# Optimization experiments

Measured on AMD Instinct MI355X. Metric: run time of the kernel, lower is better.

Reference implementation:

```python
import jax, jax.numpy as jnp
import numpy as np

CONF_THRES = 0.8
NMS_THRES = 0.4
MAX_DET = 300          # fixed capacity for jit-compatible NMS output
N_BOXES = 262144
N_CLASSES = 80


def xywh2xyxy(x):
    xy, wh = x[..., :2], x[..., 2:4]
    return jnp.concatenate([xy - wh * 0.5, xy + wh * 0.5], axis=-1)


def bbox_iou(box, boxes):
    # one box [4] vs many [N,4]; original uses the +1 pixel-area convention
    x1 = jnp.maximum(box[0], boxes[:, 0])
    y1 = jnp.maximum(box[1], boxes[:, 1])
    x2 = jnp.minimum(box[2], boxes[:, 2])
    y2 = jnp.minimum(box[3], boxes[:, 3])
    inter = jnp.clip(x2 - x1 + 1, 0) * jnp.clip(y2 - y1 + 1, 0)
    a1 = (box[2] - box[0] + 1) * (box[3] - box[1] + 1)
    a2 = (boxes[:, 2] - boxes[:, 0] + 1) * (boxes[:, 3] - boxes[:, 1] + 1)
    return inter / (a1 + a2 - inter + 1e-16)


def nms_single(pred):
    # pred: [N, 85] raw YOLO output for one image
    boxes = xywh2xyxy(pred[:, :4])
    obj = pred[:, 4]
    cls_scores = pred[:, 5:]
    class_conf = cls_scores.max(axis=-1)
    class_pred = jnp.argmax(cls_scores, axis=-1).astype(pred.dtype)
    valid = obj >= CONF_THRES
    score = obj * class_conf
    # sort valid boxes by descending score; invalid pushed to the end
    order = jnp.argsort(jnp.where(valid, -score, jnp.inf))
    det = jnp.concatenate(
        [boxes, obj[:, None], class_conf[:, None], class_pred[:, None]], axis=1
    )[order]  # [N, 7] = x1,y1,x2,y2,obj,class_conf,class_pred
    valid = valid[order]

    def step(valid, _):
        idx = jnp.argmax(valid)            # first still-valid (= highest score)
        any_valid = jnp.any(valid)
        cur = det[idx]
        iou = bbox_iou(cur[:4], det[:, :4])
        invalid = (iou > NMS_THRES) & (det[:, 6] == cur[6]) & valid
        # weighted box merge over the suppressed group (as in original NMS)
        w = jnp.where(invalid, det[:, 4], 0.0)
        merged = (w[:, None] * det[:, :4]).sum(0) / (w.sum() + 1e-16)
        out = jnp.where(any_valid,
                        jnp.concatenate([merged, cur[4:]]),
                        jnp.zeros(7, pred.dtype))
        return valid & ~invalid, (out, any_valid)

    _, (kept, kept_valid) = jax.lax.scan(step, valid, None, length=MAX_DET)
    return kept, kept_valid  # [MAX_DET,7], [MAX_DET]


def setup_inputs() -> dict:
    key = jax.random.key(0)
    detections = jax.random.uniform(key, (1, N_BOXES, 5 + N_CLASSES), dtype=jnp.float32)
    return {"detections": detections}


def reference(detections):
    kept, kv = nms_single(detections[0])
    d = kept[:, 5:]                        # [MAX_DET, 2] = (class_conf, class_pred)
    conf_key = jnp.where(kv, d[:, 0], -jnp.inf)  # padded rows sort to the end
    order = jnp.argsort(conf_key)          # ascending (torch argsort)
    d = d[order][::-1]                     # torch.flip -> descending class_conf
    kv = kv[order][::-1]
    probs = jnp.where(kv, d[:, 0], 0.0)    # self.probs
    ids = d[:, 1][None, :]                 # self.ids, shape [1, MAX_DET]
    return ids, probs
```

## Files before the change

kernel.cpp:

```cpp
#include <hip/hip_runtime.h>

#pragma clang fp contract(off)

#define NBOX 262144
#define NCLS 80
#define ROWS 85
#define CAP 1024
#define NSUB 8
#define SUBCAP 128
#define POOL 8192
#define BPT 2
#define S1BOX 512

typedef unsigned long long ull;

__global__ __launch_bounds__(1024) void k_init(int* __restrict__ cnt_pad,
                                               int* __restrict__ pool_count,
                                               int* __restrict__ done_count) {
    const int t = threadIdx.x;
    for (int i = t; i < NCLS * NSUB * 16; i += 1024) cnt_pad[i] = 0;
    if (t == 0) { *pool_count = 0; *done_count = 0; }
}

__global__ __launch_bounds__(256) void k_stage1(const float* __restrict__ det,
                                                int* __restrict__ cnt_pad,
                                                ull* __restrict__ key2,
                                                float* __restrict__ conf2,
                                                float4* __restrict__ box2) {
    __shared__ int s_wl[S1BOX];
    __shared__ float s_obj[S1BOX];
    __shared__ int s_nv;
    const int t = threadIdx.x;
    const int b0 = blockIdx.x * S1BOX;
    const int sb = blockIdx.x & (NSUB - 1);

    if (t == 0) s_nv = 0;
    __syncthreads();

    float obj[BPT];
    #pragma unroll
    for (int i = 0; i < BPT; i++)
        obj[i] = det[(size_t)(b0 + (i << 8) + t) * ROWS + 4];
    #pragma unroll
    for (int i = 0; i < BPT; i++) {
        if (obj[i] >= 0.8f) {
            int r = atomicAdd(&s_nv, 1);
            s_wl[r] = (i << 8) + t;
            s_obj[r] = obj[i];
        }
    }
    __syncthreads();
    const int nv = s_nv;

    const int grp = t >> 4, c = t & 15;
    const int lane = t & 63;
    #pragma unroll 2
    for (int r0 = 0; r0 < nv; r0 += 16) {
        int widx = r0 + grp;
        if (widx < nv) {
            int b = s_wl[widx];
            const float* p = det + (size_t)(b0 + b) * ROWS;
            float aux = (c < 5) ? p[c] : 0.0f;
            float v0 = p[5 + c];
            float v1 = p[21 + c];
            float v2 = p[37 + c];
            float v3 = p[53 + c];
            float v4 = p[69 + c];
            float mv = v0; int mj = c;
            if (v1 > mv) { mv = v1; mj = 16 + c; }
            if (v2 > mv) { mv = v2; mj = 32 + c; }
            if (v3 > mv) { mv = v3; mj = 48 + c; }
            if (v4 > mv) { mv = v4; mj = 64 + c; }
            #pragma unroll
            for (int off = 8; off; off >>= 1) {
                float ov = __shfl_xor(mv, off);
                int oj = __shfl_xor(mj, off);
                if (ov > mv || (ov == mv && oj < mj)) { mv = ov; mj = oj; }
            }
            int gb = lane & 48;
            float x = __shfl(aux, gb + 0);
            float y = __shfl(aux, gb + 1);
            float w = __shfl(aux, gb + 2);
            float h = __shfl(aux, gb + 3);
            if (c == 0) {
                float ob = s_obj[widx];
                float score = ob * mv;
                float hw = w * 0.5f, hh = h * 0.5f;
                int gi = b0 + b;
                int r = atomicAdd(&cnt_pad[((mj * NSUB + sb) << 4)], 1);
                if (r < SUBCAP) {
                    int pos = (mj << 10) + (sb << 7) + r;
                    key2[pos] = ((ull)(~__float_as_uint(score)) << 32) | (unsigned)gi;
                    conf2[pos] = mv;
                    box2[pos] = make_float4(x - hw, y - hh, x + hw, y + hh);
                }
            }
        }
    }
}

__device__ __forceinline__ int exact_alive16(ull (&k)[16]) {
    int a = 0;
    #pragma unroll
    for (int j = 0; j < 16; j++) a += (int)__popcll(__ballot(k[j] != ~0ULL));
    return a;
}

__device__ __forceinline__ void bsort512(ull (&x)[8], int lane) {
    #pragma unroll
    for (int k = 2; k <= 512; k <<= 1) {
        #pragma unroll
        for (int j = k >> 1; j >= 64; j >>= 1) {
            const int jr = j >> 6;
            #pragma unroll
            for (int r2 = 0; r2 < 8; r2++) {
                if ((r2 & jr) == 0) {
                    const bool asc = (((r2 << 6) & k) == 0);
                    ull a = x[r2], b = x[r2 | jr];
                    if ((a > b) == asc) { x[r2] = b; x[r2 | jr] = a; }
                }
            }
        }
        #pragma unroll
        for (int j = ((k >> 1) > 32 ? 32 : (k >> 1)); j >= 1; j >>= 1) {
            #pragma unroll
            for (int r2 = 0; r2 < 8; r2++) {
                int i = (r2 << 6) + lane;
                bool asc = ((i & k) == 0);
                ull o = __shfl_xor(x[r2], j);
                bool lower = ((lane & j) == 0);
                ull mn = x[r2] < o ? x[r2] : o;
                ull mx2 = x[r2] < o ? o : x[r2];
                x[r2] = (asc == lower) ? mn : mx2;
            }
        }
    }
}

__global__ __launch_bounds__(256) void k_nmsfinal(const int* __restrict__ cnt_pad,
                                                  const ull* __restrict__ key2,
                                                  const float* __restrict__ conf2,
                                                  const float4* __restrict__ box2,
                                                  ull* __restrict__ pool_key,
                                                  float* __restrict__ pool_conf,
                                                  int* __restrict__ pool_cls,
                                                  int* __restrict__ pool_count,
                                                  int* __restrict__ done_count,
                                                  float* __restrict__ out) {
    __shared__ float s_x1[CAP], s_y1[CAP], s_x2[CAP], s_y2[CAP];
    __shared__ float s_area[CAP], s_conf[CAP];
    __shared__ ull s_key[CAP];
    __shared__ int s_cnt[NSUB];
    __shared__ ull pkey[304];
    __shared__ float pconf[304];
    __shared__ int s_fin;
    __shared__ int s_hist[256];
    __shared__ int s_wt[4];
    __shared__ int s_stat[4];
    __shared__ ull s_buf[512];
    __shared__ unsigned s_cb[512];
    __shared__ unsigned s_cl[512];

    const int c = blockIdx.x, t = threadIdx.x, lane = t & 63, wave = t >> 6;
    const int s0 = c << 10;

    ull rk[4]; float4 rb[4]; float rc[4];
    #pragma unroll
    for (int i = 0; i < 4; i++) {
        int pos = t + (i << 8);
        rk[i] = key2[s0 + pos];
        rb[i] = box2[s0 + pos];
        rc[i] = conf2[s0 + pos];
    }
    if (t < NSUB) s_cnt[t] = min(cnt_pad[((c * NSUB + t) << 4)], SUBCAP);
    __syncthreads();
    #pragma unroll
    for (int i = 0; i < 4; i++) {
        int pos = t + (i << 8);
        bool ok = (pos & (SUBCAP - 1)) < s_cnt[pos >> 7];
        float4 b = ok ? rb[i] : make_float4(0.f, 0.f, 0.f, 0.f);
        s_key[pos] = ok ? rk[i] : ~0ULL;
        s_x1[pos] = b.x; s_y1[pos] = b.y; s_x2[pos] = b.z; s_y2[pos] = b.w;
        s_area[pos] = (b.z - b.x + 1.0f) * (b.w - b.y + 1.0f);
        s_conf[pos] = ok ? rc[i] : 0.0f;
    }
    __syncthreads();

    if (wave == 0) {
        int cv0 = 0;
        if (lane < NSUB) cv0 = s_cnt[lane];
        int ntot = cv0;
        #pragma unroll
        for (int off = 32; off; off >>= 1) ntot += __shfl_xor(ntot, off);

        ull k16[16];
        #pragma unroll
        for (int j = 0; j < 16; j++) k16[j] = s_key[(j << 6) + lane];

        int alive = ntot, np = 0;
        while (alive > 0 && np < 300) {
            ull v8[8]; int i8[8];
            #pragma unroll
            for (int j = 0; j < 8; j++) {
                bool l = k16[j + 8] < k16[j];
                v8[j] = l ? k16[j + 8] : k16[j];
                i8[j] = l ? j + 8 : j;
            }
            #pragma unroll
            for (int j = 0; j < 4; j++) {
                if (v8[j + 4] < v8[j]) { v8[j] = v8[j + 4]; i8[j] = i8[j + 4]; }
            }
            if (v8[2] < v8[0]) { v8[0] = v8[2]; i8[0] = i8[2]; }
            if (v8[3] < v8[1]) { v8[1] = v8[3]; i8[1] = i8[3]; }
            if (v8[1] < v8[0]) { v8[0] = v8[1]; i8[0] = i8[1]; }
            ull lm = v8[0]; const int lj = i8[0];

            unsigned lo = (unsigned)lm;
            unsigned hi = (unsigned)(lm >> 32);
            unsigned mh = hi;
            #pragma unroll
            for (int off = 32; off; off >>= 1) {
                unsigned o = __shfl_xor(mh, off);
                mh = o < mh ? o : mh;
            }
            ull wb = __ballot(hi == mh);
            ull gm; int wl2;
            if (mh == 0xFFFFFFFFu || __popcll(wb) != 1) {
                ull g = (hi == mh) ? lm : ~0ULL;
                #pragma unroll
                for (int off = 32; off; off >>= 1) {
                    ull o = __shfl_xor(g, off);
                    if (o < g) g = o;
                }
                gm = g;
                if (gm == ~0ULL) { alive = 0; break; }
                wb = __ballot(lm == gm);
                wl2 = (int)__ffsll((long long)wb) - 1;
            } else {
                wl2 = (int)__ffsll((long long)wb) - 1;
                gm = ((ull)mh << 32) | (ull)__shfl(lo, wl2);
            }
            int wpos = __shfl((lj << 6) + lane, wl2);
            float cx1 = s_x1[wpos], cy1 = s_y1[wpos];
            float cx2 = s_x2[wpos], cy2 = s_y2[wpos];
            float a1 = s_area[wpos];
            if (lane == 0) { pkey[np] = gm; pconf[np] = s_conf[wpos]; }
            np++;
            #pragma unroll
            for (int j = 0; j < 16; j++) {
                if (k16[j] != ~0ULL) {
                    int pos = (j << 6) + lane;
                    float xx1 = fmaxf(cx1, s_x1[pos]), yy1 = fmaxf(cy1, s_y1[pos]);
                    float xx2 = fminf(cx2, s_x2[pos]), yy2 = fminf(cy2, s_y2[pos]);
                    float iw = xx2 - xx1 + 1.0f, ih = yy2 - yy1 + 1.0f;
                    float inter = fmaxf(iw, 0.0f) * fmaxf(ih, 0.0f);
                    float iou = inter / (a1 + s_area[pos] - inter + 1e-16f);
                    if (iou > 0.4f) k16[j] = ~0ULL;
                }
            }
            if ((np & 7) == 0) alive = exact_alive16(k16);
        }

        int npw = min(np, 300);
        int base = 0;
        if (lane == 0 && npw) base = atomicAdd(pool_count, npw);
        base = __shfl(base, 0);
        for (int j = lane; j < npw; j += 64) {
            int pp = base + j;
            if (pp < POOL) {
                ull gm = pkey[j];
                ull pk = ((ull)((unsigned)(gm >> 32) & 0x7FFFFFFFu) << 32)
                       | ((gm & 0xFFFFFFFFull) << 14) | (ull)pp;
                __hip_atomic_store(&pool_key[pp], pk,
                                   __ATOMIC_RELAXED, __HIP_MEMORY_SCOPE_AGENT);
                __hip_atomic_store(&pool_conf[pp], pconf[j],
                                   __ATOMIC_RELAXED, __HIP_MEMORY_SCOPE_AGENT);
                __hip_atomic_store(&pool_cls[pp], c,
                                   __ATOMIC_RELAXED, __HIP_MEMORY_SCOPE_AGENT);
            }
        }
        asm volatile("s_waitcnt vmcnt(0)" ::: "memory");
    }
    __syncthreads();
    if (t == 0) {
        int ticket = atomicAdd(done_count, 1);
        s_fin = (ticket == NCLS - 1) ? 1 : 0;
    }
    __syncthreads();
    if (!s_fin) return;

    const int K = min(__hip_atomic_load(pool_count, __ATOMIC_RELAXED,
                                        __HIP_MEMORY_SCOPE_AGENT), POOL);
    ull key[32];
    #pragma unroll
    for (int j = 0; j < 32; j++) {
        int pos = t + (j << 8);
        key[j] = (pos < K) ? __hip_atomic_load(&pool_key[pos], __ATOMIC_RELAXED,
                                               __HIP_MEMORY_SCOPE_AGENT)
                           : ~0ULL;
    }

    const bool selAll = (K <= 511);
    int sh = 55;
    ull pfin = 0;
    if (!selAll) {
        ull p = 0;
        int gBelow = 0, r = 300;
        while (true) {
            s_hist[t] = 0;
            __syncthreads();
            #pragma unroll
            for (int j = 0; j < 32; j++) {
                ull kk = key[j];
                if ((kk >> (sh + 8)) == p)
                    atomicAdd(&s_hist[(int)((kk >> sh) & 0xFFull)], 1);
            }
            __syncthreads();
            int v = s_hist[t];
            int incv = v;
            for (int off = 1; off < 64; off <<= 1) {
                int o = __shfl_up(incv, off);
                if (lane >= off) incv += o;
            }
            if (lane == 63) s_wt[wave] = incv;
            __syncthreads();
            int wo = 0;
            #pragma unroll
            for (int w2 = 0; w2 < 4; w2++) if (w2 < wave) wo += s_wt[w2];
            int cumIncl = wo + incv;
            int cumExcl = cumIncl - v;
            if (cumExcl < r && r <= cumIncl) {
                s_stat[0] = t; s_stat[1] = cumExcl; s_stat[2] = cumIncl;
            }
            __syncthreads();
            int D = s_stat[0], below = s_stat[1], incl = s_stat[2];
            if (gBelow + incl <= 511 || sh == 7) {
                pfin = (p << 8) | (ull)D;
                break;
            }
            p = (p << 8) | (ull)D;
            gBelow += below;
            r = 300 - gBelow;
            sh -= 8;
            __syncthreads();
        }
    }

    if (t == 0) s_stat[3] = 0;
    __syncthreads();
    int ci = 0;
    #pragma unroll
    for (int j = 0; j < 32; j++) {
        ull kk = key[j];
        bool sel = selAll ? ((kk >> 63) == 0) : ((kk >> sh) <= pfin);
        if (sel) ci++;
    }
    int inc = ci;
    for (int off = 1; off < 64; off <<= 1) {
        int o = __shfl_up(inc, off);
        if (lane >= off) inc += o;
    }
    int wtot = __shfl(inc, 63);
    int wbase2 = 0;
    if (lane == 0 && wtot) wbase2 = atomicAdd(&s_stat[3], wtot);
    wbase2 = __shfl(wbase2, 0);
    int wp = wbase2 + inc - ci;
    #pragma unroll
    for (int j = 0; j < 32; j++) {
        ull kk = key[j];
        bool sel = selAll ? ((kk >> 63) == 0) : ((kk >> sh) <= pfin);
        if (sel) s_buf[wp++] = kk;
    }
    __syncthreads();
    const int S = s_stat[3];
    for (int i = t; i < 512; i += 256) if (i >= S) s_buf[i] = ~0ULL;
    __syncthreads();
    if (wave != 0) return;

    #pragma clang loop unroll(disable)
    for (int pass = 0; pass < 2; pass++) {
        ull x[8];
        #pragma unroll
        for (int r2 = 0; r2 < 8; r2++) x[r2] = s_buf[(r2 << 6) + lane];
        bsort512(x, lane);
        if (pass == 0) {
            #pragma unroll
            for (int r2 = 0; r2 < 8; r2++) {
                int i = (r2 << 6) + lane;
                ull kk = x[r2];
                ull k2 = ~0ULL;
                if (i < 300 && kk != ~0ULL) {
                    int pidx = (int)(kk & 0x3FFFull);
                    unsigned cb = __float_as_uint(
                        __hip_atomic_load(&pool_conf[pidx], __ATOMIC_RELAXED,
                                          __HIP_MEMORY_SCOPE_AGENT));
                    unsigned cl = (unsigned)__hip_atomic_load(&pool_cls[pidx],
                                          __ATOMIC_RELAXED, __HIP_MEMORY_SCOPE_AGENT);
                    s_cb[i] = cb; s_cl[i] = cl;
                    k2 = ((ull)(~cb) << 32) | (unsigned)(~i);
                }
                s_buf[i] = k2;
            }
        } else {
            #pragma unroll
            for (int r2 = 0; r2 < 8; r2++) {
                int i = (r2 << 6) + lane;
                if (i < 300) {
                    ull kk = x[r2];
                    float idv = 0.0f, pv = 0.0f;
                    if (kk != ~0ULL) {
                        int slot = (int)(~(unsigned)(kk & 0xFFFFFFFFull));
                        pv = __uint_as_float(s_cb[slot]);
                        idv = (float)(int)s_cl[slot];
                    }
                    out[i] = idv;
                    out[300 + i] = pv;
                }
            }
        }
    }
}

extern "C" void kernel_launch(void* const* d_in, const int* in_sizes, int n_in,
                              void* d_out, int out_size, void* d_ws, size_t ws_size,
                              hipStream_t stream) {
    const float* det = (const float*)d_in[0];
    float* out = (float*)d_out;
    char* ws = (char*)d_ws;

    int* cnt_pad = (int*)(ws + 0);
    int* pool_count = (int*)(ws + 40960);
    int* done_count = (int*)(ws + 40964);
    ull* key2 = (ull*)(ws + 41024);
    float* conf2 = (float*)(ws + 696384);
    float4* box2 = (float4*)(ws + 1024064);
    ull* pool_key = (ull*)(ws + 2334784);
    float* pool_conf = (float*)(ws + 2400320);
    int* pool_cls = (int*)(ws + 2433088);

    k_init<<<1, 1024, 0, stream>>>(cnt_pad, pool_count, done_count);
    k_stage1<<<NBOX / S1BOX, 256, 0, stream>>>(det, cnt_pad, key2, conf2, box2);
    k_nmsfinal<<<NCLS, 256, 0, stream>>>(cnt_pad, key2, conf2, box2,
                                         pool_key, pool_conf, pool_cls, pool_count,
                                         done_count, out);
}
```

Before: 178.2 us.

## Spread per-class greedy NMS across all four waves with register-resident boxes

The per-class greedy NMS loop, which previously ran on a single wave over 1024 candidates held in shared memory, now runs on all four waves. Each lane keeps four candidates' keys and boxes in registers, and waves exchange their local winners through shared memory every iteration. This cuts per-wave IoU work fourfold and removes the shared-memory box arrays. In exchange, each iteration pays two block-wide barriers. The periodic alive-count check is dropped, so the loop ends when the block minimum becomes the sentinel.

```diff
diff --git a/kernel.cpp b/kernel.cpp
--- a/kernel.cpp
+++ b/kernel.cpp
@@ -99,13 +99,6 @@
     }
 }
 
-__device__ __forceinline__ int exact_alive16(ull (&k)[16]) {
-    int a = 0;
-    #pragma unroll
-    for (int j = 0; j < 16; j++) a += (int)__popcll(__ballot(k[j] != ~0ULL));
-    return a;
-}
-
 __device__ __forceinline__ void bsort512(ull (&x)[8], int lane) {
     #pragma unroll
     for (int k = 2; k <= 512; k <<= 1) {
@@ -147,13 +140,13 @@
                                                   int* __restrict__ pool_count,
                                                   int* __restrict__ done_count,
                                                   float* __restrict__ out) {
-    __shared__ float s_x1[CAP], s_y1[CAP], s_x2[CAP], s_y2[CAP];
-    __shared__ float s_area[CAP], s_conf[CAP];
-    __shared__ ull s_key[CAP];
     __shared__ int s_cnt[NSUB];
+    __shared__ ull s_wkey[4];
+    __shared__ float s_wbox[4][6];
+    __shared__ int s_base;
+    __shared__ int s_fin;
     __shared__ ull pkey[304];
     __shared__ float pconf[304];
-    __shared__ int s_fin;
     __shared__ int s_hist[256];
     __shared__ int s_wt[4];
     __shared__ int s_stat[4];
@@ -164,123 +157,109 @@
     const int c = blockIdx.x, t = threadIdx.x, lane = t & 63, wave = t >> 6;
     const int s0 = c << 10;
 
-    ull rk[4]; float4 rb[4]; float rc[4];
-    #pragma unroll
-    for (int i = 0; i < 4; i++) {
-        int pos = t + (i << 8);
-        rk[i] = key2[s0 + pos];
-        rb[i] = box2[s0 + pos];
-        rc[i] = conf2[s0 + pos];
+    ull k4[4]; float x1[4], y1[4], x2[4], y2[4], ar[4], cf[4];
+    #pragma unroll
+    for (int j = 0; j < 4; j++) {
+        int pos = (wave << 8) + (j << 6) + lane;
+        k4[j] = key2[s0 + pos];
+        float4 b = box2[s0 + pos];
+        x1[j] = b.x; y1[j] = b.y; x2[j] = b.z; y2[j] = b.w;
+        cf[j] = conf2[s0 + pos];
     }
     if (t < NSUB) s_cnt[t] = min(cnt_pad[((c * NSUB + t) << 4)], SUBCAP);
     __syncthreads();
     #pragma unroll
-    for (int i = 0; i < 4; i++) {
-        int pos = t + (i << 8);
+    for (int j = 0; j < 4; j++) {
+        int pos = (wave << 8) + (j << 6) + lane;
         bool ok = (pos & (SUBCAP - 1)) < s_cnt[pos >> 7];
-        float4 b = ok ? rb[i] : make_float4(0.f, 0.f, 0.f, 0.f);
-        s_key[pos] = ok ? rk[i] : ~0ULL;
-        s_x1[pos] = b.x; s_y1[pos] = b.y; s_x2[pos] = b.z; s_y2[pos] = b.w;
-        s_area[pos] = (b.z - b.x + 1.0f) * (b.w - b.y + 1.0f);
-        s_conf[pos] = ok ? rc[i] : 0.0f;
-    }
-    __syncthreads();
-
-    if (wave == 0) {
-        int cv0 = 0;
-        if (lane < NSUB) cv0 = s_cnt[lane];
-        int ntot = cv0;
-        #pragma unroll
-        for (int off = 32; off; off >>= 1) ntot += __shfl_xor(ntot, off);
-
-        ull k16[16];
-        #pragma unroll
-        for (int j = 0; j < 16; j++) k16[j] = s_key[(j << 6) + lane];
-
-        int alive = ntot, np = 0;
-        while (alive > 0 && np < 300) {
-            ull v8[8]; int i8[8];
-            #pragma unroll
-            for (int j = 0; j < 8; j++) {
-                bool l = k16[j + 8] < k16[j];
-                v8[j] = l ? k16[j + 8] : k16[j];
-                i8[j] = l ? j + 8 : j;
-            }
-            #pragma unroll
-            for (int j = 0; j < 4; j++) {
-                if (v8[j + 4] < v8[j]) { v8[j] = v8[j + 4]; i8[j] = i8[j + 4]; }
-            }
-            if (v8[2] < v8[0]) { v8[0] = v8[2]; i8[0] = i8[2]; }
-            if (v8[3] < v8[1]) { v8[1] = v8[3]; i8[1] = i8[3]; }
-            if (v8[1] < v8[0]) { v8[0] = v8[1]; i8[0] = i8[1]; }
-            ull lm = v8[0]; const int lj = i8[0];
-
-            unsigned lo = (unsigned)lm;
-            unsigned hi = (unsigned)(lm >> 32);
-            unsigned mh = hi;
+        if (!ok) {
+            k4[j] = ~0ULL;
+            x1[j] = 0.f; y1[j] = 0.f; x2[j] = 0.f; y2[j] = 0.f; cf[j] = 0.f;
+        }
+        ar[j] = (x2[j] - x1[j] + 1.0f) * (y2[j] - y1[j] + 1.0f);
+    }
+
+    int np = 0;
+    while (np < 300) {
+        ull va = k4[0]; int ia = 0;
+        if (k4[1] < va) { va = k4[1]; ia = 1; }
+        ull vb = k4[2]; int ib = 2;
+        if (k4[3] < vb) { vb = k4[3]; ib = 3; }
+        ull lm = va; int lj = ia;
+        if (vb < va) { lm = vb; lj = ib; }
+        unsigned lo = (unsigned)lm;
+        unsigned hi = (unsigned)(lm >> 32);
+        unsigned mh = hi;
+        #pragma unroll
+        for (int off = 32; off; off >>= 1) {
+            unsigned o = __shfl_xor(mh, off);
+            mh = o < mh ? o : mh;
+        }
+        ull wb = __ballot(hi == mh);
+        ull wm; int wl;
+        if (__popcll(wb) != 1) {
+            ull g = (hi == mh) ? lm : ~0ULL;
             #pragma unroll
             for (int off = 32; off; off >>= 1) {
-                unsigned o = __shfl_xor(mh, off);
-                mh = o < mh ? o : mh;
-            }
-            ull wb = __ballot(hi == mh);
-            ull gm; int wl2;
-            if (mh == 0xFFFFFFFFu || __popcll(wb) != 1) {
-                ull g = (hi == mh) ? lm : ~0ULL;
-                #pragma unroll
-                for (int off = 32; off; off >>= 1) {
-                    ull o = __shfl_xor(g, off);
-                    if (o < g) g = o;
-                }
-                gm = g;
-                if (gm == ~0ULL) { alive = 0; break; }
-                wb = __ballot(lm == gm);
-                wl2 = (int)__ffsll((long long)wb) - 1;
-            } else {
-                wl2 = (int)__ffsll((long long)wb) - 1;
-                gm = ((ull)mh << 32) | (ull)__shfl(lo, wl2);
-            }
-            int wpos = __shfl((lj << 6) + lane, wl2);
-            float cx1 = s_x1[wpos], cy1 = s_y1[wpos];
-            float cx2 = s_x2[wpos], cy2 = s_y2[wpos];
-            float a1 = s_area[wpos];
-            if (lane == 0) { pkey[np] = gm; pconf[np] = s_conf[wpos]; }
-            np++;
-            #pragma unroll
-            for (int j = 0; j < 16; j++) {
-                if (k16[j] != ~0ULL) {
-                    int pos = (j << 6) + lane;
-                    float xx1 = fmaxf(cx1, s_x1[pos]), yy1 = fmaxf(cy1, s_y1[pos]);
-                    float xx2 = fminf(cx2, s_x2[pos]), yy2 = fminf(cy2, s_y2[pos]);
-                    float iw = xx2 - xx1 + 1.0f, ih = yy2 - yy1 + 1.0f;
-                    float inter = fmaxf(iw, 0.0f) * fmaxf(ih, 0.0f);
-                    float iou = inter / (a1 + s_area[pos] - inter + 1e-16f);
-                    if (iou > 0.4f) k16[j] = ~0ULL;
-                }
-            }
-            if ((np & 7) == 0) alive = exact_alive16(k16);
-        }
-
-        int npw = min(np, 300);
-        int base = 0;
-        if (lane == 0 && npw) base = atomicAdd(pool_count, npw);
-        base = __shfl(base, 0);
-        for (int j = lane; j < npw; j += 64) {
-            int pp = base + j;
-            if (pp < POOL) {
-                ull gm = pkey[j];
-                ull pk = ((ull)((unsigned)(gm >> 32) & 0x7FFFFFFFu) << 32)
-                       | ((gm & 0xFFFFFFFFull) << 14) | (ull)pp;
-                __hip_atomic_store(&pool_key[pp], pk,
-                                   __ATOMIC_RELAXED, __HIP_MEMORY_SCOPE_AGENT);
-                __hip_atomic_store(&pool_conf[pp], pconf[j],
-                                   __ATOMIC_RELAXED, __HIP_MEMORY_SCOPE_AGENT);
-                __hip_atomic_store(&pool_cls[pp], c,
-                                   __ATOMIC_RELAXED, __HIP_MEMORY_SCOPE_AGENT);
-            }
-        }
-        asm volatile("s_waitcnt vmcnt(0)" ::: "memory");
-    }
+                ull o = __shfl_xor(g, off);
+                if (o < g) g = o;
+            }
+            wm = g;
+            wb = __ballot(lm == wm);
+            wl = (int)__ffsll((long long)wb) - 1;
+        } else {
+            wl = (int)__ffsll((long long)wb) - 1;
+            wm = ((ull)mh << 32) | (ull)__shfl(lo, wl);
+        }
+        if (lane == wl) {
+            s_wkey[wave] = wm;
+            s_wbox[wave][0] = x1[lj]; s_wbox[wave][1] = y1[lj];
+            s_wbox[wave][2] = x2[lj]; s_wbox[wave][3] = y2[lj];
+            s_wbox[wave][4] = ar[lj]; s_wbox[wave][5] = cf[lj];
+        }
+        __syncthreads();
+        ull gk = s_wkey[0]; int gw = 0;
+        #pragma unroll
+        for (int w2 = 1; w2 < 4; w2++) {
+            ull kk = s_wkey[w2];
+            if (kk < gk) { gk = kk; gw = w2; }
+        }
+        if (gk == ~0ULL) break;
+        float cx1 = s_wbox[gw][0], cy1 = s_wbox[gw][1];
+        float cx2 = s_wbox[gw][2], cy2 = s_wbox[gw][3];
+        float a1 = s_wbox[gw][4];
+        if (t == 0) { pkey[np] = gk; pconf[np] = s_wbox[gw][5]; }
+        np++;
+        #pragma unroll
+        for (int j = 0; j < 4; j++) {
+            float xx1 = fmaxf(cx1, x1[j]), yy1 = fmaxf(cy1, y1[j]);
+            float xx2 = fminf(cx2, x2[j]), yy2 = fminf(cy2, y2[j]);
+            float iw = xx2 - xx1 + 1.0f, ih = yy2 - yy1 + 1.0f;
+            float inter = fmaxf(iw, 0.0f) * fmaxf(ih, 0.0f);
+            float iou = inter / (a1 + ar[j] - inter + 1e-16f);
+            if (iou > 0.4f) k4[j] = ~0ULL;
+        }
+        __syncthreads();
+    }
+
+    const int npw = np;
+    if (t == 0 && npw) s_base = atomicAdd(pool_count, npw);
+    __syncthreads();
+    for (int j = t; j < npw; j += 256) {
+        int pp = s_base + j;
+        if (pp < POOL) {
+            ull gm = pkey[j];
+            ull pk = ((ull)((unsigned)(gm >> 32) & 0x7FFFFFFFu) << 32)
+                   | ((gm & 0xFFFFFFFFull) << 14) | (ull)pp;
+            __hip_atomic_store(&pool_key[pp], pk,
+                               __ATOMIC_RELAXED, __HIP_MEMORY_SCOPE_AGENT);
+            __hip_atomic_store(&pool_conf[pp], pconf[j],
+                               __ATOMIC_RELAXED, __HIP_MEMORY_SCOPE_AGENT);
+            __hip_atomic_store(&pool_cls[pp], c,
+                               __ATOMIC_RELAXED, __HIP_MEMORY_SCOPE_AGENT);
+        }
+    }
+    asm volatile("s_waitcnt vmcnt(0)" ::: "memory");
     __syncthreads();
     if (t == 0) {
         int ticket = atomicAdd(done_count, 1);
```

Result: faster. 170.8 us (-4.2%).
